# Kernel tuning notes

Hardware: AMD Instinct MI355X
Metric: run time of the kernel (lower is better)

The kernel has to match this reference:

```python
import jax, jax.numpy as jnp
import numpy as np

N, F_IN, H, C, E = 50000, 256, 4, 64, 800000
HC = H * C  # n_target_nodes = 256


def setup_inputs() -> dict:
    key = jax.random.key(0)
    ks = jax.random.split(key, 16)
    s = 1.0 / np.sqrt(F_IN)
    inp = {
        "x": jax.random.normal(ks[0], (N, F_IN), jnp.float32),
        "edge_index": jax.random.randint(ks[1], (2, E), 0, N, jnp.int64),
        "edge_attr": jax.random.uniform(ks[2], (E, 1), jnp.float32),
        "Wq": jax.random.normal(ks[3], (F_IN, HC), jnp.float32) * s,
        "bq": jnp.zeros((HC,), jnp.float32),
        "Wk": jax.random.normal(ks[4], (F_IN, HC), jnp.float32) * s,
        "bk": jnp.zeros((HC,), jnp.float32),
        "Wv": jax.random.normal(ks[5], (F_IN, HC), jnp.float32) * s,
        "bv": jnp.zeros((HC,), jnp.float32),
        "We": jax.random.normal(ks[6], (1, HC), jnp.float32),
        "be": jnp.zeros((HC,), jnp.float32),
        "Wskip": jax.random.normal(ks[7], (F_IN, HC), jnp.float32) * s,
        "bskip": jnp.zeros((HC,), jnp.float32),
        "gn_weight": jnp.ones((HC,), jnp.float32),
        "gn_bias": jnp.zeros((HC,), jnp.float32),
        "gn_mean_scale": jnp.ones((HC,), jnp.float32),
    }
    return inp


def _la_forward(x, edge_index, edge_attr, Wq, bq, Wk, bk, Wv, bv, We, be,
                Wskip, bskip, gn_weight, gn_bias, gn_mean_scale):
    n = x.shape[0]
    src, dst = edge_index[0], edge_index[1]  # message src(j) -> dst(i)
    q = (x @ Wq + bq).reshape(n, H, C)
    k = (x @ Wk + bk).reshape(n, H, C)
    v = (x @ Wv + bv).reshape(n, H, C)
    e = (edge_attr @ We + be).reshape(-1, H, C)  # [E,H,C]

    k_j = k[src] + e                              # [E,H,C]
    alpha = jnp.einsum('ehc,ehc->eh', q[dst], k_j) / jnp.sqrt(jnp.float32(C))
    # edge-softmax over incoming edges of each dst node
    amax = jax.ops.segment_max(alpha, dst, num_segments=n)      # [N,H]
    ex = jnp.exp(alpha - amax[dst])
    denom = jax.ops.segment_sum(ex, dst, num_segments=n)        # [N,H]
    attn = ex / (denom[dst] + 1e-16)                            # [E,H]

    msg = (v[src] + e) * attn[:, :, None]                       # [E,H,C]
    out = jax.ops.segment_sum(msg, dst, num_segments=n).reshape(n, HC)
    out = out + x @ Wskip + bskip                               # root/skip

    # GraphNorm (single graph batch)
    mean = out.mean(axis=0)
    centered = out - gn_mean_scale * mean
    var = (centered * centered).mean(axis=0)
    out = centered / jnp.sqrt(var + 1e-5) * gn_weight + gn_bias

    out = jax.nn.relu(out)
    xt = out.T @ out                                            # [HC,HC]
    xt_min, xt_max = jnp.min(xt), jnp.max(xt)
    xt = (xt - xt_min) / (xt_max - xt_min + 1e-8)
    return xt


def reference(x, edge_index, edge_attr, Wq, bq, Wk, bk, Wv, bv, We, be,
              Wskip, bskip, gn_weight, gn_bias, gn_mean_scale):
    return _la_forward(x, edge_index, edge_attr, Wq, bq, Wk, bk, Wv, bv,
                       We, be, Wskip, bskip, gn_weight, gn_bias, gn_mean_scale)
```

## Files before the change

### kernel.cpp

```cpp
#include <hip/hip_runtime.h>
#include <math.h>


typedef float f32x4 __attribute__((ext_vector_type(4)));
typedef short s16x8 __attribute__((ext_vector_type(8)));

static __device__ __forceinline__ unsigned short f2bf(float f) {
    unsigned int u = __float_as_uint(f);
    unsigned int r = u + 0x7FFFu + ((u >> 16) & 1u);
    return (unsigned short)(r >> 16);
}
static __device__ __forceinline__ float bf2f(unsigned short u) {
    return __uint_as_float(((unsigned int)u) << 16);
}
static __device__ __forceinline__ float blo(unsigned int u) {
    return __uint_as_float(u << 16);
}
static __device__ __forceinline__ float bhi(unsigned int u) {
    return __uint_as_float(u & 0xffff0000u);
}

#define LOG2E_8 0.18033688011112042f

__global__ void la_x2bf(const float* __restrict__ x, unsigned short* __restrict__ xb,
                        int total4)
{
    int i = blockIdx.x * blockDim.x + threadIdx.x;
    int stride = gridDim.x * blockDim.x;
    for (; i < total4; i += stride) {
        float4 v = ((const float4*)x)[i];
        ushort4 o;
        o.x = f2bf(v.x); o.y = f2bf(v.y); o.z = f2bf(v.z); o.w = f2bf(v.w);
        ((ushort4*)xb)[i] = o;
    }
}

__global__ void la_wprep(const float* __restrict__ Wq, const float* __restrict__ Wk,
                         const float* __restrict__ Wv, const float* __restrict__ Ws,
                         const float* __restrict__ bq, const float* __restrict__ bk,
                         const float* __restrict__ bv, const float* __restrict__ bs,
                         unsigned short* __restrict__ wt, float* __restrict__ bcat)
{
    int col = blockIdx.x;
    int m = col >> 8, c = col & 255;
    const float* W = (m == 0) ? Wq : (m == 1) ? Wk : (m == 2) ? Wv : Ws;
    const float* B = (m == 0) ? bq : (m == 1) ? bk : (m == 2) ? bv : bs;
    int t = threadIdx.x;
    wt[(size_t)col * 256 + t] = f2bf(W[(size_t)t * 256 + c]);
    if (t == 0) bcat[col] = B[c];
}

__global__ __launch_bounds__(256) void la_gemm_mfma(
    const unsigned short* __restrict__ xb, const unsigned short* __restrict__ wt,
    const float* __restrict__ bcat,
    unsigned short* __restrict__ qarr, unsigned short* __restrict__ kv,
    unsigned short* __restrict__ skiparr, int n)
{
    __shared__ __align__(16) unsigned short As[128 * 40];
    __shared__ __align__(16) unsigned short Bs[128 * 40];

    const int row0 = blockIdx.x * 128;
    const int col0 = blockIdx.y * 128;
    const int msel = blockIdx.y >> 1;
    const int t = threadIdx.x;
    const int l = t & 63;
    const int w = t >> 6;
    const int wr = w >> 1, wc = w & 1;
    const int l15 = l & 15, l4 = l >> 4;

    f32x4 acc[4][4];
#pragma unroll
    for (int i = 0; i < 4; ++i)
#pragma unroll
        for (int j = 0; j < 4; ++j) acc[i][j] = (f32x4){0.f, 0.f, 0.f, 0.f};

    for (int k0 = 0; k0 < 256; k0 += 32) {
#pragma unroll
        for (int c2 = 0; c2 < 2; ++c2) {
            int chunk = t + c2 * 256;
            int r  = chunk >> 2;
            int ko = (chunk & 3) * 8;
            int ga = row0 + r;
            s16x8 va = (s16x8){0,0,0,0,0,0,0,0};
            if (ga < n) va = *(const s16x8*)(xb + (size_t)ga * 256 + k0 + ko);
            *(s16x8*)(As + r * 40 + ko) = va;
            int gb = col0 + r;
            s16x8 vb = *(const s16x8*)(wt + (size_t)gb * 256 + k0 + ko);
            *(s16x8*)(Bs + r * 40 + ko) = vb;
        }
        __syncthreads();
        s16x8 af[4], bfr[4];
#pragma unroll
        for (int f = 0; f < 4; ++f) {
            af[f]  = *(const s16x8*)(As + (wr * 64 + f * 16 + l15) * 40 + l4 * 8);
            bfr[f] = *(const s16x8*)(Bs + (wc * 64 + f * 16 + l15) * 40 + l4 * 8);
        }
#pragma unroll
        for (int fm = 0; fm < 4; ++fm)
#pragma unroll
            for (int fn = 0; fn < 4; ++fn)
                acc[fm][fn] = __builtin_amdgcn_mfma_f32_16x16x32_bf16(
                    af[fm], bfr[fn], acc[fm][fn], 0, 0, 0);
        __syncthreads();
    }

#pragma unroll
    for (int fm = 0; fm < 4; ++fm) {
#pragma unroll
        for (int fn = 0; fn < 4; ++fn) {
            int gc = col0 + wc * 64 + fn * 16 + l15;
            int c  = gc & 255;
            float bb = bcat[gc];
#pragma unroll
            for (int j = 0; j < 4; ++j) {
                int gr = row0 + wr * 64 + fm * 16 + l4 * 4 + j;
                if (gr >= n) continue;
                unsigned short val = f2bf(acc[fm][fn][j] + bb);
                if (msel == 0) {
                    qarr[(size_t)gr * 256 + c] = val;
                } else if (msel == 3) {
                    skiparr[(size_t)gr * 256 + c] = val;
                } else {
                    int hh = c >> 6, ch = c & 63;
                    size_t idx = (size_t)gr * 512 + hh * 128 + (ch >> 2) * 8
                               + (ch & 3) + ((msel == 2) ? 4 : 0);
                    kv[idx] = val;
                }
            }
        }
    }
}

__global__ void la_hist(const int* __restrict__ dst, int e, int* __restrict__ deg)
{
    int i = blockIdx.x * blockDim.x + threadIdx.x;
    int stride = gridDim.x * blockDim.x;
    for (; i < e; i += stride) atomicAdd(&deg[dst[i]], 1);
}

__global__ void la_chunksum(const int* __restrict__ deg, int n, int* __restrict__ part)
{
    int b = blockIdx.x, t = threadIdx.x;
    int i = b * 256 + t;
    int v = (i < n) ? deg[i] : 0;
#pragma unroll
    for (int mask = 32; mask >= 1; mask >>= 1) v += __shfl_xor(v, mask);
    __shared__ int ws[4];
    if ((t & 63) == 0) ws[t >> 6] = v;
    __syncthreads();
    if (t == 0) part[b] = ws[0] + ws[1] + ws[2] + ws[3];
}

__global__ void la_scanpart(int* __restrict__ part, int nb)
{
    __shared__ int s[256];
    int t = threadIdx.x;
    int v = (t < nb) ? part[t] : 0;
    int orig = v;
    s[t] = v;
    __syncthreads();
    for (int o = 1; o < 256; o <<= 1) {
        int u = (t >= o) ? s[t - o] : 0;
        __syncthreads();
        s[t] += u;
        __syncthreads();
    }
    if (t < nb) part[t] = s[t] - orig;
}

__global__ void la_scanfinal(const int* __restrict__ deg, int n,
                             const int* __restrict__ part, int* __restrict__ offs,
                             int* __restrict__ cursor, int e)
{
    int b = blockIdx.x, t = threadIdx.x;
    int i = b * 256 + t;
    int d = (i < n) ? deg[i] : 0;
    int v = d;
#pragma unroll
    for (int o = 1; o < 64; o <<= 1) {
        int u = __shfl_up(v, o);
        if ((t & 63) >= o) v += u;
    }
    __shared__ int wt[4];
    if ((t & 63) == 63) wt[t >> 6] = v;
    __syncthreads();
    int add = 0;
    for (int wv = 0; wv < (t >> 6); ++wv) add += wt[wv];
    int excl = v + add - d + part[b];
    if (i < n) { offs[i] = excl; cursor[i] = excl; }
    if (b == 0 && t == 0) offs[n] = e;
}

__global__ void la_scatter(const int* __restrict__ src, const int* __restrict__ dst,
                           const float* __restrict__ ea, int e,
                           int* __restrict__ cursor, uint2* __restrict__ rec)
{
    int i = blockIdx.x * blockDim.x + threadIdx.x;
    int stride = gridDim.x * blockDim.x;
    for (; i < e; i += stride) {
        int d = dst[i];
        int pos = atomicAdd(&cursor[d], 1);
        rec[pos] = make_uint2((unsigned int)src[i], __float_as_uint(ea[i]));
    }
}

__global__ __launch_bounds__(256) void la_attn3(
    const unsigned short* __restrict__ qarr,
    const unsigned short* __restrict__ kv,
    const unsigned short* __restrict__ skiparr,
    const uint2* __restrict__ rec,
    const int* __restrict__ offs,
    const float* __restrict__ We, const float* __restrict__ be,
    float* __restrict__ outb)
{
    const int node = blockIdx.x;
    const int t = threadIdx.x;
    const int h = t >> 6;
    const int l = t & 63;
    const int quarter = l >> 4;
    const int lc = l & 15;
    const int cb = h * 64 + lc * 4;

    uint2 qp = *(const uint2*)(qarr + (size_t)node * 256 + cb);
    const float q0 = blo(qp.x), q1 = bhi(qp.x);
    const float q2 = blo(qp.y), q3 = bhi(qp.y);
    float4 we4 = *(const float4*)(We + cb);
    float4 be4 = *(const float4*)(be + cb);

    float pw = fmaf(q3, we4.w, fmaf(q2, we4.z, fmaf(q1, we4.y, q0 * we4.x)));
    float pb = fmaf(q3, be4.w, fmaf(q2, be4.z, fmaf(q1, be4.y, q0 * be4.x)));
#pragma unroll
    for (int mask = 1; mask <= 8; mask <<= 1) {
        pw += __shfl_xor(pw, mask);
        pb += __shfl_xor(pb, mask);
    }
    const float qWe8 = pw * LOG2E_8;
    const float qbe8 = pb * LOG2E_8;

    const int start = offs[node], end = offs[node + 1];
    const int koff = h * 128 + lc * 8;

    float lsum = 0.f, Sfa = 0.f;
    float a0 = 0.f, a1 = 0.f, a2 = 0.f, a3 = 0.f;

    for (int j0 = start; j0 < end; j0 += 4) {
        int j = j0 + quarter;
        bool valid = (j < end);
        int jj = valid ? j : j0;
        uint2 r = rec[jj];
        int   s   = (int)r.x;
        float eaj = __uint_as_float(r.y);
        uint4 kvu = *(const uint4*)(kv + (((size_t)s) << 9) + koff);
        float k0 = blo(kvu.x), k1 = bhi(kvu.x);
        float k2 = blo(kvu.y), k3 = bhi(kvu.y);
        float d = fmaf(q3, k3, fmaf(q2, k2, fmaf(q1, k1, q0 * k0)));
#pragma unroll
        for (int mask = 1; mask <= 8; mask <<= 1) d += __shfl_xor(d, mask);
        float aL = fmaf(d, LOG2E_8, fmaf(eaj, qWe8, qbe8));
        aL = valid ? aL : -INFINITY;
        float f = exp2f(aL);
        lsum += f;
        Sfa = fmaf(f, eaj, Sfa);
        float v0 = blo(kvu.z), v1 = bhi(kvu.z);
        float v2 = blo(kvu.w), v3 = bhi(kvu.w);
        a0 = fmaf(f, v0, a0);
        a1 = fmaf(f, v1, a1);
        a2 = fmaf(f, v2, a2);
        a3 = fmaf(f, v3, a3);
    }

#pragma unroll
    for (int mask = 16; mask <= 32; mask <<= 1) {
        lsum += __shfl_xor(lsum, mask);
        Sfa  += __shfl_xor(Sfa,  mask);
        a0   += __shfl_xor(a0,   mask);
        a1   += __shfl_xor(a1,   mask);
        a2   += __shfl_xor(a2,   mask);
        a3   += __shfl_xor(a3,   mask);
    }

    if (quarter == 0) {
        float inv = 1.f / (lsum + 1e-16f);
        uint2 sp = *(const uint2*)(skiparr + (size_t)node * 256 + cb);
        float4 o;
        o.x = fmaf(we4.x, Sfa, fmaf(be4.x, lsum, a0)) * inv + blo(sp.x);
        o.y = fmaf(we4.y, Sfa, fmaf(be4.y, lsum, a1)) * inv + bhi(sp.x);
        o.z = fmaf(we4.z, Sfa, fmaf(be4.z, lsum, a2)) * inv + blo(sp.y);
        o.w = fmaf(we4.w, Sfa, fmaf(be4.w, lsum, a3)) * inv + bhi(sp.y);
        *(float4*)(outb + (size_t)node * 256 + cb) = o;
    }
}

__global__ __launch_bounds__(256) void la_colsum(
    const float* __restrict__ outb, float* __restrict__ cs,
    float* __restrict__ cs2, int n)
{
    const int col = threadIdx.x;
    const int r0 = blockIdx.x * 64;
    const int rend = (r0 + 64 < n) ? r0 + 64 : n;
    float s = 0.f, s2 = 0.f;
    for (int r = r0; r < rend; ++r) {
        float vv = outb[(size_t)r * 256 + col];
        s += vv;
        s2 = fmaf(vv, vv, s2);
    }
    atomicAdd(&cs[col], s);
    atomicAdd(&cs2[col], s2);
}

__global__ void la_coeff(const float* __restrict__ cs, const float* __restrict__ cs2,
                         const float* __restrict__ gnw, const float* __restrict__ gnb,
                         const float* __restrict__ gms,
                         float* __restrict__ A, float* __restrict__ B, int n)
{
    int j = threadIdx.x;
    float invn = 1.f / (float)n;
    float mean = cs[j] * invn;
    float m2   = cs2[j] * invn;
    float s    = gms[j];
    float var  = m2 - 2.f * s * mean * mean + s * s * mean * mean;
    float inv  = 1.f / sqrtf(var + 1e-5f);
    float a    = gnw[j] * inv;
    A[j] = a;
    B[j] = gnb[j] - s * mean * a;
}

__global__ __launch_bounds__(256) void la_gram_mfma(
    const float* __restrict__ outb, const float* __restrict__ A,
    const float* __restrict__ B, float* __restrict__ xt, int n, int kchunk)
{
    __shared__ __align__(16) unsigned int Ta[128 * 20];
    __shared__ __align__(16) unsigned int Tb[128 * 20];

    const int bx = blockIdx.x;
    const int kc   = bx / 3;
    const int tile = bx - kc * 3;
    const int i0 = (tile == 2) ? 128 : 0;
    const int j0 = (tile == 0) ? 0 : 128;
    const bool diag = (tile != 1);
    const int kbeg = kc * kchunk;
    if (kbeg >= n) return;
    const int kend = (kbeg + kchunk < n) ? kbeg + kchunk : n;

    const int t = threadIdx.x;
    const int l = t & 63, w = t >> 6;
    const int wr = w >> 1, wc = w & 1;
    const int l15 = l & 15, l4 = l >> 4;

    const int kp  = t >> 4;
    const int cg8 = t & 15;

    float Ai[8], Bi[8], Aj[8], Bj[8];
#pragma unroll
    for (int u = 0; u < 2; ++u) {
        float4 a = *(const float4*)(A + i0 + cg8 * 8 + u * 4);
        float4 b = *(const float4*)(B + i0 + cg8 * 8 + u * 4);
        Ai[u*4+0]=a.x; Ai[u*4+1]=a.y; Ai[u*4+2]=a.z; Ai[u*4+3]=a.w;
        Bi[u*4+0]=b.x; Bi[u*4+1]=b.y; Bi[u*4+2]=b.z; Bi[u*4+3]=b.w;
        float4 a2 = *(const float4*)(A + j0 + cg8 * 8 + u * 4);
        float4 b2 = *(const float4*)(B + j0 + cg8 * 8 + u * 4);
        Aj[u*4+0]=a2.x; Aj[u*4+1]=a2.y; Aj[u*4+2]=a2.z; Aj[u*4+3]=a2.w;
        Bj[u*4+0]=b2.x; Bj[u*4+1]=b2.y; Bj[u*4+2]=b2.z; Bj[u*4+3]=b2.w;
    }

    f32x4 acc[4][4];
#pragma unroll
    for (int i = 0; i < 4; ++i)
#pragma unroll
        for (int j = 0; j < 4; ++j) acc[i][j] = (f32x4){0.f, 0.f, 0.f, 0.f};

    const int nsteps = (kend - kbeg + 31) >> 5;
    for (int ks = 0; ks < nsteps; ++ks) {
        const int gr0 = kbeg + ks * 32 + kp * 2;
        const bool v0 = (gr0 < kend), v1 = (gr0 + 1 < kend);

        {
            float r0[8], r1[8];
            float4 xa = make_float4(0,0,0,0), xb4 = make_float4(0,0,0,0);
            float4 ya = make_float4(0,0,0,0), yb4 = make_float4(0,0,0,0);
            if (v0) {
                xa  = *(const float4*)(outb + (size_t)gr0 * 256 + i0 + cg8 * 8);
                xb4 = *(const float4*)(outb + (size_t)gr0 * 256 + i0 + cg8 * 8 + 4);
            }
            if (v1) {
                ya  = *(const float4*)(outb + (size_t)(gr0+1) * 256 + i0 + cg8 * 8);
                yb4 = *(const float4*)(outb + (size_t)(gr0+1) * 256 + i0 + cg8 * 8 + 4);
            }
            float xs[8] = {xa.x,xa.y,xa.z,xa.w,xb4.x,xb4.y,xb4.z,xb4.w};
            float ys[8] = {ya.x,ya.y,ya.z,ya.w,yb4.x,yb4.y,yb4.z,yb4.w};
#pragma unroll
            for (int j = 0; j < 8; ++j) {
                r0[j] = v0 ? fmaxf(fmaf(xs[j], Ai[j], Bi[j]), 0.f) : 0.f;
                r1[j] = v1 ? fmaxf(fmaf(ys[j], Ai[j], Bi[j]), 0.f) : 0.f;
            }
#pragma unroll
            for (int j = 0; j < 8; ++j) {
                int c = cg8 * 8 + j;
                unsigned int u = (unsigned int)f2bf(r0[j])
                               | ((unsigned int)f2bf(r1[j]) << 16);
                Ta[c * 20 + (kp ^ (((c >> 3) & 3) << 2))] = u;
            }
        }
        if (!diag) {
            float r0[8], r1[8];
            float4 xa = make_float4(0,0,0,0), xb4 = make_float4(0,0,0,0);
            float4 ya = make_float4(0,0,0,0), yb4 = make_float4(0,0,0,0);
            if (v0) {
                xa  = *(const float4*)(outb + (size_t)gr0 * 256 + j0 + cg8 * 8);
                xb4 = *(const float4*)(outb + (size_t)gr0 * 256 + j0 + cg8 * 8 + 4);
            }
            if (v1) {
                ya  = *(const float4*)(outb + (size_t)(gr0+1) * 256 + j0 + cg8 * 8);
                yb4 = *(const float4*)(outb + (size_t)(gr0+1) * 256 + j0 + cg8 * 8 + 4);
            }
            float xs[8] = {xa.x,xa.y,xa.z,xa.w,xb4.x,xb4.y,xb4.z,xb4.w};
            float ys[8] = {ya.x,ya.y,ya.z,ya.w,yb4.x,yb4.y,yb4.z,yb4.w};
#pragma unroll
            for (int j = 0; j < 8; ++j) {
                r0[j] = v0 ? fmaxf(fmaf(xs[j], Aj[j], Bj[j]), 0.f) : 0.f;
                r1[j] = v1 ? fmaxf(fmaf(ys[j], Aj[j], Bj[j]), 0.f) : 0.f;
            }
#pragma unroll
            for (int j = 0; j < 8; ++j) {
                int c = cg8 * 8 + j;
                unsigned int u = (unsigned int)f2bf(r0[j])
                               | ((unsigned int)f2bf(r1[j]) << 16);
                Tb[c * 20 + (kp ^ (((c >> 3) & 3) << 2))] = u;
            }
        }
        __syncthreads();

        const unsigned int* TB = diag ? Ta : Tb;
        s16x8 af[4], bfr[4];
#pragma unroll
        for (int f = 0; f < 4; ++f) {
            int ca = wr * 64 + f * 16 + l15;
            af[f] = *(const s16x8*)(Ta + ca * 20 + ((l4 * 4) ^ (((ca >> 3) & 3) << 2)));
            int cb2 = wc * 64 + f * 16 + l15;
            bfr[f] = *(const s16x8*)(TB + cb2 * 20 + ((l4 * 4) ^ (((cb2 >> 3) & 3) << 2)));
        }
#pragma unroll
        for (int fm = 0; fm < 4; ++fm)
#pragma unroll
            for (int fn = 0; fn < 4; ++fn)
                acc[fm][fn] = __builtin_amdgcn_mfma_f32_16x16x32_bf16(
                    af[fm], bfr[fn], acc[fm][fn], 0, 0, 0);
        __syncthreads();
    }

#pragma unroll
    for (int fm = 0; fm < 4; ++fm)
#pragma unroll
        for (int fn = 0; fn < 4; ++fn) {
            int col = j0 + wc * 64 + fn * 16 + l15;
#pragma unroll
            for (int j = 0; j < 4; ++j) {
                int row = i0 + wr * 64 + fm * 16 + l4 * 4 + j;
                float vv = acc[fm][fn][j];
                atomicAdd(&xt[(size_t)row * 256 + col], vv);
                if (tile == 1)
                    atomicAdd(&xt[(size_t)col * 256 + row], vv);
            }
        }
}

__global__ __launch_bounds__(256) void la_minmax_part(
    const float* __restrict__ xt, float* __restrict__ mmp)
{
    const int b = blockIdx.x, t = threadIdx.x;
    float mn = INFINITY, mx = -INFINITY;
#pragma unroll
    for (int k = 0; k < 2; ++k) {
        float4 v = ((const float4*)xt)[b * 512 + k * 256 + t];
        mn = fminf(mn, fminf(fminf(v.x, v.y), fminf(v.z, v.w)));
        mx = fmaxf(mx, fmaxf(fmaxf(v.x, v.y), fmaxf(v.z, v.w)));
    }
#pragma unroll
    for (int mask = 32; mask >= 1; mask >>= 1) {
        mn = fminf(mn, __shfl_xor(mn, mask));
        mx = fmaxf(mx, __shfl_xor(mx, mask));
    }
    __shared__ float smn[4], smx[4];
    if ((t & 63) == 0) { smn[t >> 6] = mn; smx[t >> 6] = mx; }
    __syncthreads();
    if (t == 0) {
        mn = fminf(fminf(smn[0], smn[1]), fminf(smn[2], smn[3]));
        mx = fmaxf(fmaxf(smx[0], smx[1]), fmaxf(smx[2], smx[3]));
        mmp[b * 2]     = mn;
        mmp[b * 2 + 1] = mx;
    }
}

__global__ void la_norm(float* __restrict__ xt, const float* __restrict__ mmp)
{
    float mn = INFINITY, mx = -INFINITY;
#pragma unroll
    for (int i = 0; i < 32; ++i) {
        mn = fminf(mn, mmp[i * 2]);
        mx = fmaxf(mx, mmp[i * 2 + 1]);
    }
    float inv = 1.f / (mx - mn + 1e-8f);
    int i = blockIdx.x * blockDim.x + threadIdx.x;
    xt[i] = (xt[i] - mn) * inv;
}

extern "C" void kernel_launch(void* const* d_in, const int* in_sizes, int n_in,
                              void* d_out, int out_size, void* d_ws, size_t ws_size,
                              hipStream_t stream)
{
    const float* x   = (const float*)d_in[0];
    const int*   ei  = (const int*)  d_in[1];
    const float* ea  = (const float*)d_in[2];
    const float* Wq  = (const float*)d_in[3];
    const float* bq  = (const float*)d_in[4];
    const float* Wk  = (const float*)d_in[5];
    const float* bk  = (const float*)d_in[6];
    const float* Wv  = (const float*)d_in[7];
    const float* bv  = (const float*)d_in[8];
    const float* We  = (const float*)d_in[9];
    const float* be  = (const float*)d_in[10];
    const float* Ws  = (const float*)d_in[11];
    const float* bs  = (const float*)d_in[12];
    const float* gnw = (const float*)d_in[13];
    const float* gnb = (const float*)d_in[14];
    const float* gms = (const float*)d_in[15];

    const int n = in_sizes[0] / 256;
    const int e = in_sizes[1] / 2;
    const int* srcI = ei;
    const int* dstI = ei + e;

    char* ws = (char*)d_ws;
    size_t off = 0;
    auto take = [&](size_t bytes) -> void* {
        void* p = (void*)(ws + off);
        off += (bytes + 255) & ~(size_t)255;
        return p;
    };
    unsigned short* xb    = (unsigned short*)take((size_t)n * 256 * 2);
    unsigned short* wtbuf = (unsigned short*)take((size_t)1024 * 256 * 2);
    float*          bcat  = (float*)take(1024 * 4);
    unsigned short* qarr  = (unsigned short*)take((size_t)n * 256 * 2);
    unsigned short* kv    = (unsigned short*)take((size_t)n * 512 * 2);
    unsigned short* skipb = (unsigned short*)take((size_t)n * 256 * 2);
    float* outb   = (float*)take((size_t)n * 256 * 4);
    int*   deg    = (int*)  take((size_t)n * 4);
    int*   cursor = (int*)  take((size_t)n * 4);
    int*   offs   = (int*)  take((size_t)(n + 1) * 4);
    int*   part   = (int*)  take(256 * 4);
    uint2* csrR   = (uint2*)take((size_t)e * 8);
    float* cs     = (float*)take(256 * 4);
    float* cs2    = (float*)take(256 * 4);
    float* cA     = (float*)take(256 * 4);
    float* cB     = (float*)take(256 * 4);
    float* mmp    = (float*)take(64 * 4);
    (void)ws_size; (void)n_in; (void)out_size;

    float* xt = (float*)d_out;

    hipMemsetAsync(deg, 0, (size_t)n * 4, stream);
    hipMemsetAsync(cs,  0, 256 * 4, stream);
    hipMemsetAsync(cs2, 0, 256 * 4, stream);
    hipMemsetAsync(xt,  0, (size_t)65536 * 4, stream);

    la_x2bf <<<2048, 256, 0, stream>>>(x, xb, n * 64);
    la_wprep<<<1024, 256, 0, stream>>>(Wq, Wk, Wv, Ws, bq, bk, bv, bs, wtbuf, bcat);

    dim3 gg((n + 127) / 128, 8);
    la_gemm_mfma<<<gg, 256, 0, stream>>>(xb, wtbuf, bcat, qarr, kv, skipb, n);

    const int nchunk = (n + 255) / 256;
    la_hist     <<<1024, 256, 0, stream>>>(dstI, e, deg);
    la_chunksum <<<nchunk, 256, 0, stream>>>(deg, n, part);
    la_scanpart <<<1, 256, 0, stream>>>(part, nchunk);
    la_scanfinal<<<nchunk, 256, 0, stream>>>(deg, n, part, offs, cursor, e);
    la_scatter  <<<1024, 256, 0, stream>>>(srcI, dstI, ea, e, cursor, csrR);

    la_attn3<<<n, 256, 0, stream>>>(qarr, kv, skipb, csrR, offs, We, be, outb);

    la_colsum<<<(n + 63) / 64, 256, 0, stream>>>(outb, cs, cs2, n);
    la_coeff <<<1, 256, 0, stream>>>(cs, cs2, gnw, gnb, gms, cA, cB, n);

    const int KSPLIT = 64;
    int kchunk = ((n + KSPLIT - 1) / KSPLIT + 31) & ~31;
    la_gram_mfma<<<3 * KSPLIT, 256, 0, stream>>>(outb, cA, cB, xt, n, kchunk);

    la_minmax_part<<<32, 256, 0, stream>>>(xt, mmp);
    la_norm<<<256, 256, 0, stream>>>(xt, mmp);
}
```

Baseline: 461.4 us.

## Fuse x-to-bf16 conversion into GEMM, store attention output as bf16, fold GraphNorm coeffs

Removes the separate x→bf16 pass by having the projection GEMM load fp32 x rows, convert them and keep a 64-row bf16 tile resident in LDS while looping over all 1024 output columns. The weight transpose is rebuilt as a tiled LDS transpose with far fewer blocks. The attention output buffer becomes bf16, halving traffic for colsum and the Gram kernel, and the GraphNorm coefficient kernel is folded into the Gram kernel. The costs are extra rounding of the pre-norm activations and a GEMM with fewer, longer-running blocks that each restage B tiles eight times.

New measurement: 492.1 us. 1.07x slower.

```diff
diff --git a/kernel.cpp b/kernel.cpp
--- a/kernel.cpp
+++ b/kernel.cpp
@@ -22,109 +22,134 @@
 
 #define LOG2E_8 0.18033688011112042f
 
-__global__ void la_x2bf(const float* __restrict__ x, unsigned short* __restrict__ xb,
-                        int total4)
-{
-    int i = blockIdx.x * blockDim.x + threadIdx.x;
-    int stride = gridDim.x * blockDim.x;
-    for (; i < total4; i += stride) {
-        float4 v = ((const float4*)x)[i];
-        ushort4 o;
-        o.x = f2bf(v.x); o.y = f2bf(v.y); o.z = f2bf(v.z); o.w = f2bf(v.w);
-        ((ushort4*)xb)[i] = o;
-    }
-}
-
-__global__ void la_wprep(const float* __restrict__ Wq, const float* __restrict__ Wk,
-                         const float* __restrict__ Wv, const float* __restrict__ Ws,
-                         const float* __restrict__ bq, const float* __restrict__ bk,
-                         const float* __restrict__ bv, const float* __restrict__ bs,
-                         unsigned short* __restrict__ wt, float* __restrict__ bcat)
-{
-    int col = blockIdx.x;
-    int m = col >> 8, c = col & 255;
+__global__ __launch_bounds__(256) void la_wprep2(
+    const float* __restrict__ Wq, const float* __restrict__ Wk,
+    const float* __restrict__ Wv, const float* __restrict__ Ws,
+    const float* __restrict__ bq, const float* __restrict__ bk,
+    const float* __restrict__ bv, const float* __restrict__ bs,
+    unsigned short* __restrict__ wt, float* __restrict__ bcat)
+{
+    __shared__ float T[64][68];
+    const int bid = blockIdx.x;
+    const int m  = bid >> 4;
+    const int kt = (bid >> 2) & 3, ct = bid & 3;
+    const int k0 = kt * 64, c0 = ct * 64;
     const float* W = (m == 0) ? Wq : (m == 1) ? Wk : (m == 2) ? Wv : Ws;
     const float* B = (m == 0) ? bq : (m == 1) ? bk : (m == 2) ? bv : bs;
-    int t = threadIdx.x;
-    wt[(size_t)col * 256 + t] = f2bf(W[(size_t)t * 256 + c]);
-    if (t == 0) bcat[col] = B[c];
-}
-
-__global__ __launch_bounds__(256) void la_gemm_mfma(
-    const unsigned short* __restrict__ xb, const unsigned short* __restrict__ wt,
+    const int t = threadIdx.x;
+
+#pragma unroll
+    for (int it = 0; it < 4; ++it) {
+        int s = it * 256 + t;
+        int r = s >> 4;
+        int q = (s & 15) * 4;
+        float4 v = *(const float4*)(W + (size_t)(k0 + r) * 256 + c0 + q);
+        T[r][q + 0] = v.x; T[r][q + 1] = v.y;
+        T[r][q + 2] = v.z; T[r][q + 3] = v.w;
+    }
+    __syncthreads();
+#pragma unroll
+    for (int it = 0; it < 4; ++it) {
+        int s = it * 256 + t;
+        int c = s >> 4;
+        int kq = (s & 15) * 4;
+        ushort4 o;
+        o.x = f2bf(T[kq + 0][c]); o.y = f2bf(T[kq + 1][c]);
+        o.z = f2bf(T[kq + 2][c]); o.w = f2bf(T[kq + 3][c]);
+        *(ushort4*)(wt + (size_t)(m * 256 + c0 + c) * 256 + k0 + kq) = o;
+    }
+    if (kt == 0 && t < 64) bcat[m * 256 + c0 + t] = B[c0 + t];
+}
+
+__global__ __launch_bounds__(256) void la_gemm2(
+    const float* __restrict__ x, const unsigned short* __restrict__ wt,
     const float* __restrict__ bcat,
     unsigned short* __restrict__ qarr, unsigned short* __restrict__ kv,
     unsigned short* __restrict__ skiparr, int n)
 {
-    __shared__ __align__(16) unsigned short As[128 * 40];
+    __shared__ __align__(16) unsigned short As[64 * 264];
     __shared__ __align__(16) unsigned short Bs[128 * 40];
 
-    const int row0 = blockIdx.x * 128;
-    const int col0 = blockIdx.y * 128;
-    const int msel = blockIdx.y >> 1;
+    const int row0 = blockIdx.x * 64;
     const int t = threadIdx.x;
-    const int l = t & 63;
-    const int w = t >> 6;
-    const int wr = w >> 1, wc = w & 1;
+    const int l = t & 63, w = t >> 6;
+    const int wr = w & 1, wc = w >> 1;
     const int l15 = l & 15, l4 = l >> 4;
 
-    f32x4 acc[4][4];
-#pragma unroll
-    for (int i = 0; i < 4; ++i)
-#pragma unroll
-        for (int j = 0; j < 4; ++j) acc[i][j] = (f32x4){0.f, 0.f, 0.f, 0.f};
-
-    for (int k0 = 0; k0 < 256; k0 += 32) {
-#pragma unroll
-        for (int c2 = 0; c2 < 2; ++c2) {
-            int chunk = t + c2 * 256;
-            int r  = chunk >> 2;
-            int ko = (chunk & 3) * 8;
-            int ga = row0 + r;
-            s16x8 va = (s16x8){0,0,0,0,0,0,0,0};
-            if (ga < n) va = *(const s16x8*)(xb + (size_t)ga * 256 + k0 + ko);
-            *(s16x8*)(As + r * 40 + ko) = va;
-            int gb = col0 + r;
-            s16x8 vb = *(const s16x8*)(wt + (size_t)gb * 256 + k0 + ko);
-            *(s16x8*)(Bs + r * 40 + ko) = vb;
-        }
-        __syncthreads();
-        s16x8 af[4], bfr[4];
-#pragma unroll
-        for (int f = 0; f < 4; ++f) {
-            af[f]  = *(const s16x8*)(As + (wr * 64 + f * 16 + l15) * 40 + l4 * 8);
-            bfr[f] = *(const s16x8*)(Bs + (wc * 64 + f * 16 + l15) * 40 + l4 * 8);
-        }
-#pragma unroll
-        for (int fm = 0; fm < 4; ++fm)
-#pragma unroll
-            for (int fn = 0; fn < 4; ++fn)
-                acc[fm][fn] = __builtin_amdgcn_mfma_f32_16x16x32_bf16(
-                    af[fm], bfr[fn], acc[fm][fn], 0, 0, 0);
-        __syncthreads();
-    }
-
-#pragma unroll
-    for (int fm = 0; fm < 4; ++fm) {
-#pragma unroll
-        for (int fn = 0; fn < 4; ++fn) {
-            int gc = col0 + wc * 64 + fn * 16 + l15;
-            int c  = gc & 255;
-            float bb = bcat[gc];
-#pragma unroll
-            for (int j = 0; j < 4; ++j) {
-                int gr = row0 + wr * 64 + fm * 16 + l4 * 4 + j;
-                if (gr >= n) continue;
-                unsigned short val = f2bf(acc[fm][fn][j] + bb);
-                if (msel == 0) {
-                    qarr[(size_t)gr * 256 + c] = val;
-                } else if (msel == 3) {
-                    skiparr[(size_t)gr * 256 + c] = val;
-                } else {
-                    int hh = c >> 6, ch = c & 63;
-                    size_t idx = (size_t)gr * 512 + hh * 128 + (ch >> 2) * 8
-                               + (ch & 3) + ((msel == 2) ? 4 : 0);
-                    kv[idx] = val;
+#pragma unroll
+    for (int it = 0; it < 16; ++it) {
+        int s = it * 256 + t;
+        int r = s >> 6;
+        int q = (s & 63) * 4;
+        int gr = row0 + r;
+        float4 v = make_float4(0.f, 0.f, 0.f, 0.f);
+        if (gr < n) v = *(const float4*)(x + (size_t)gr * 256 + q);
+        ushort4 o;
+        o.x = f2bf(v.x); o.y = f2bf(v.y); o.z = f2bf(v.z); o.w = f2bf(v.w);
+        *(ushort4*)(As + r * 264 + q) = o;
+    }
+    __syncthreads();
+
+    for (int p = 0; p < 8; ++p) {
+        const int col0 = p * 128;
+        const int msel = p >> 1;
+        f32x4 acc[2][4];
+#pragma unroll
+        for (int i = 0; i < 2; ++i)
+#pragma unroll
+            for (int j = 0; j < 4; ++j) acc[i][j] = (f32x4){0.f, 0.f, 0.f, 0.f};
+
+        for (int ks = 0; ks < 8; ++ks) {
+            const int k0 = ks * 32;
+#pragma unroll
+            for (int it = 0; it < 2; ++it) {
+                int s = it * 256 + t;
+                int c = s >> 2;
+                int ko = (s & 3) * 8;
+                *(s16x8*)(Bs + c * 40 + ko) =
+                    *(const s16x8*)(wt + (size_t)(col0 + c) * 256 + k0 + ko);
+            }
+            __syncthreads();
+            s16x8 af[2], bfr[4];
+#pragma unroll
+            for (int f = 0; f < 2; ++f)
+                af[f] = *(const s16x8*)(As + (wr * 32 + f * 16 + l15) * 264
+                                        + k0 + l4 * 8);
+#pragma unroll
+            for (int f = 0; f < 4; ++f)
+                bfr[f] = *(const s16x8*)(Bs + (wc * 64 + f * 16 + l15) * 40
+                                         + l4 * 8);
+#pragma unroll
+            for (int fm = 0; fm < 2; ++fm)
+#pragma unroll
+                for (int fn = 0; fn < 4; ++fn)
+                    acc[fm][fn] = __builtin_amdgcn_mfma_f32_16x16x32_bf16(
+                        af[fm], bfr[fn], acc[fm][fn], 0, 0, 0);
+            __syncthreads();
+        }
+
+#pragma unroll
+        for (int fm = 0; fm < 2; ++fm) {
+#pragma unroll
+            for (int fn = 0; fn < 4; ++fn) {
+                int gc = col0 + wc * 64 + fn * 16 + l15;
+                int c  = gc & 255;
+                float bb = bcat[gc];
+#pragma unroll
+                for (int j = 0; j < 4; ++j) {
+                    int gr = row0 + wr * 32 + fm * 16 + l4 * 4 + j;
+                    if (gr >= n) continue;
+                    unsigned short val = f2bf(acc[fm][fn][j] + bb);
+                    if (msel == 0) {
+                        qarr[(size_t)gr * 256 + c] = val;
+                    } else if (msel == 3) {
+                        skiparr[(size_t)gr * 256 + c] = val;
+                    } else {
+                        int hh = c >> 6, ch = c & 63;
+                        size_t idx = (size_t)gr * 512 + hh * 128 + (ch >> 2) * 8
+                                   + (ch & 3) + ((msel == 2) ? 4 : 0);
+                        kv[idx] = val;
+                    }
                 }
             }
         }
@@ -211,7 +236,7 @@
     const uint2* __restrict__ rec,
     const int* __restrict__ offs,
     const float* __restrict__ We, const float* __restrict__ be,
-    float* __restrict__ outb)
+    unsigned short* __restrict__ outb)
 {
     const int node = blockIdx.x;
     const int t = threadIdx.x;
@@ -282,17 +307,17 @@
     if (quarter == 0) {
         float inv = 1.f / (lsum + 1e-16f);
         uint2 sp = *(const uint2*)(skiparr + (size_t)node * 256 + cb);
-        float4 o;
-        o.x = fmaf(we4.x, Sfa, fmaf(be4.x, lsum, a0)) * inv + blo(sp.x);
-        o.y = fmaf(we4.y, Sfa, fmaf(be4.y, lsum, a1)) * inv + bhi(sp.x);
-        o.z = fmaf(we4.z, Sfa, fmaf(be4.z, lsum, a2)) * inv + blo(sp.y);
-        o.w = fmaf(we4.w, Sfa, fmaf(be4.w, lsum, a3)) * inv + bhi(sp.y);
-        *(float4*)(outb + (size_t)node * 256 + cb) = o;
+        ushort4 o;
+        o.x = f2bf(fmaf(we4.x, Sfa, fmaf(be4.x, lsum, a0)) * inv + blo(sp.x));
+        o.y = f2bf(fmaf(we4.y, Sfa, fmaf(be4.y, lsum, a1)) * inv + bhi(sp.x));
+        o.z = f2bf(fmaf(we4.z, Sfa, fmaf(be4.z, lsum, a2)) * inv + blo(sp.y));
+        o.w = f2bf(fmaf(we4.w, Sfa, fmaf(be4.w, lsum, a3)) * inv + bhi(sp.y));
+        *(ushort4*)(outb + (size_t)node * 256 + cb) = o;
     }
 }
 
 __global__ __launch_bounds__(256) void la_colsum(
-    const float* __restrict__ outb, float* __restrict__ cs,
+    const unsigned short* __restrict__ outb, float* __restrict__ cs,
     float* __restrict__ cs2, int n)
 {
     const int col = threadIdx.x;
@@ -300,7 +325,7 @@
     const int rend = (r0 + 64 < n) ? r0 + 64 : n;
     float s = 0.f, s2 = 0.f;
     for (int r = r0; r < rend; ++r) {
-        float vv = outb[(size_t)r * 256 + col];
+        float vv = bf2f(outb[(size_t)r * 256 + col]);
         s += vv;
         s2 = fmaf(vv, vv, s2);
     }
@@ -308,26 +333,12 @@
     atomicAdd(&cs2[col], s2);
 }
 
-__global__ void la_coeff(const float* __restrict__ cs, const float* __restrict__ cs2,
-                         const float* __restrict__ gnw, const float* __restrict__ gnb,
-                         const float* __restrict__ gms,
-                         float* __restrict__ A, float* __restrict__ B, int n)
-{
-    int j = threadIdx.x;
-    float invn = 1.f / (float)n;
-    float mean = cs[j] * invn;
-    float m2   = cs2[j] * invn;
-    float s    = gms[j];
-    float var  = m2 - 2.f * s * mean * mean + s * s * mean * mean;
-    float inv  = 1.f / sqrtf(var + 1e-5f);
-    float a    = gnw[j] * inv;
-    A[j] = a;
-    B[j] = gnb[j] - s * mean * a;
-}
-
 __global__ __launch_bounds__(256) void la_gram_mfma(
-    const float* __restrict__ outb, const float* __restrict__ A,
-    const float* __restrict__ B, float* __restrict__ xt, int n, int kchunk)
+    const unsigned short* __restrict__ outb,
+    const float* __restrict__ cs, const float* __restrict__ cs2,
+    const float* __restrict__ gnw, const float* __restrict__ gnb,
+    const float* __restrict__ gms,
+    float* __restrict__ xt, int n, int kchunk)
 {
     __shared__ __align__(16) unsigned int Ta[128 * 20];
     __shared__ __align__(16) unsigned int Tb[128 * 20];
@@ -350,17 +361,28 @@
     const int kp  = t >> 4;
     const int cg8 = t & 15;
 
+    const float invn = 1.f / (float)n;
     float Ai[8], Bi[8], Aj[8], Bj[8];
 #pragma unroll
-    for (int u = 0; u < 2; ++u) {
-        float4 a = *(const float4*)(A + i0 + cg8 * 8 + u * 4);
-        float4 b = *(const float4*)(B + i0 + cg8 * 8 + u * 4);
-        Ai[u*4+0]=a.x; Ai[u*4+1]=a.y; Ai[u*4+2]=a.z; Ai[u*4+3]=a.w;
-        Bi[u*4+0]=b.x; Bi[u*4+1]=b.y; Bi[u*4+2]=b.z; Bi[u*4+3]=b.w;
-        float4 a2 = *(const float4*)(A + j0 + cg8 * 8 + u * 4);
-        float4 b2 = *(const float4*)(B + j0 + cg8 * 8 + u * 4);
-        Aj[u*4+0]=a2.x; Aj[u*4+1]=a2.y; Aj[u*4+2]=a2.z; Aj[u*4+3]=a2.w;
-        Bj[u*4+0]=b2.x; Bj[u*4+1]=b2.y; Bj[u*4+2]=b2.z; Bj[u*4+3]=b2.w;
+    for (int j = 0; j < 8; ++j) {
+        {
+            int ci = i0 + cg8 * 8 + j;
+            float mean = cs[ci] * invn;
+            float m2   = cs2[ci] * invn;
+            float s    = gms[ci];
+            float var  = m2 - 2.f * s * mean * mean + s * s * mean * mean;
+            float a    = gnw[ci] / sqrtf(var + 1e-5f);
+            Ai[j] = a; Bi[j] = gnb[ci] - s * mean * a;
+        }
+        {
+            int cj = j0 + cg8 * 8 + j;
+            float mean = cs[cj] * invn;
+            float m2   = cs2[cj] * invn;
+            float s    = gms[cj];
+            float var  = m2 - 2.f * s * mean * mean + s * s * mean * mean;
+            float a    = gnw[cj] / sqrtf(var + 1e-5f);
+            Aj[j] = a; Bj[j] = gnb[cj] - s * mean * a;
+        }
     }
 
     f32x4 acc[4][4];
@@ -375,56 +397,38 @@
         const bool v0 = (gr0 < kend), v1 = (gr0 + 1 < kend);
 
         {
-            float r0[8], r1[8];
-            float4 xa = make_float4(0,0,0,0), xb4 = make_float4(0,0,0,0);
-            float4 ya = make_float4(0,0,0,0), yb4 = make_float4(0,0,0,0);
-            if (v0) {
-                xa  = *(const float4*)(outb + (size_t)gr0 * 256 + i0 + cg8 * 8);
-                xb4 = *(const float4*)(outb + (size_t)gr0 * 256 + i0 + cg8 * 8 + 4);
-            }
-            if (v1) {
-                ya  = *(const float4*)(outb + (size_t)(gr0+1) * 256 + i0 + cg8 * 8);
-                yb4 = *(const float4*)(outb + (size_t)(gr0+1) * 256 + i0 + cg8 * 8 + 4);
-            }
-            float xs[8] = {xa.x,xa.y,xa.z,xa.w,xb4.x,xb4.y,xb4.z,xb4.w};
-            float ys[8] = {ya.x,ya.y,ya.z,ya.w,yb4.x,yb4.y,yb4.z,yb4.w};
+            uint4 u0 = make_uint4(0,0,0,0), u1 = make_uint4(0,0,0,0);
+            if (v0) u0 = *(const uint4*)(outb + (size_t)gr0 * 256 + i0 + cg8 * 8);
+            if (v1) u1 = *(const uint4*)(outb + (size_t)(gr0+1) * 256 + i0 + cg8 * 8);
+            float xs[8] = {blo(u0.x),bhi(u0.x),blo(u0.y),bhi(u0.y),
+                           blo(u0.z),bhi(u0.z),blo(u0.w),bhi(u0.w)};
+            float ys[8] = {blo(u1.x),bhi(u1.x),blo(u1.y),bhi(u1.y),
+                           blo(u1.z),bhi(u1.z),blo(u1.w),bhi(u1.w)};
 #pragma unroll
             for (int j = 0; j < 8; ++j) {
-                r0[j] = v0 ? fmaxf(fmaf(xs[j], Ai[j], Bi[j]), 0.f) : 0.f;
-                r1[j] = v1 ? fmaxf(fmaf(ys[j], Ai[j], Bi[j]), 0.f) : 0.f;
-            }
-#pragma unroll
-            for (int j = 0; j < 8; ++j) {
+                float r0 = v0 ? fmaxf(fmaf(xs[j], Ai[j], Bi[j]), 0.f) : 0.f;
+                float r1 = v1 ? fmaxf(fmaf(ys[j], Ai[j], Bi[j]), 0.f) : 0.f;
                 int c = cg8 * 8 + j;
-                unsigned int u = (unsigned int)f2bf(r0[j])
-                               | ((unsigned int)f2bf(r1[j]) << 16);
+                unsigned int u = (unsigned int)f2bf(r0)
+                               | ((unsigned int)f2bf(r1) << 16);
                 Ta[c * 20 + (kp ^ (((c >> 3) & 3) << 2))] = u;
             }
         }
         if (!diag) {
-            float r0[8], r1[8];
-            float4 xa = make_float4(0,0,0,0), xb4 = make_float4(0,0,0,0);
-            float4 ya = make_float4(0,0,0,0), yb4 = make_float4(0,0,0,0);
-            if (v0) {
-                xa  = *(const float4*)(outb + (size_t)gr0 * 256 + j0 + cg8 * 8);
-                xb4 = *(const float4*)(outb + (size_t)gr0 * 256 + j0 + cg8 * 8 + 4);
-            }
-            if (v1) {
-                ya  = *(const float4*)(outb + (size_t)(gr0+1) * 256 + j0 + cg8 * 8);
-                yb4 = *(const float4*)(outb + (size_t)(gr0+1) * 256 + j0 + cg8 * 8 + 4);
-            }
-            float xs[8] = {xa.x,xa.y,xa.z,xa.w,xb4.x,xb4.y,xb4.z,xb4.w};
-            float ys[8] = {ya.x,ya.y,ya.z,ya.w,yb4.x,yb4.y,yb4.z,yb4.w};
+            uint4 u0 = make_uint4(0,0,0,0), u1 = make_uint4(0,0,0,0);
+            if (v0) u0 = *(const uint4*)(outb + (size_t)gr0 * 256 + j0 + cg8 * 8);
+            if (v1) u1 = *(const uint4*)(outb + (size_t)(gr0+1) * 256 + j0 + cg8 * 8);
+            float xs[8] = {blo(u0.x),bhi(u0.x),blo(u0.y),bhi(u0.y),
+                           blo(u0.z),bhi(u0.z),blo(u0.w),bhi(u0.w)};
+            float ys[8] = {blo(u1.x),bhi(u1.x),blo(u1.y),bhi(u1.y),
+                           blo(u1.z),bhi(u1.z),blo(u1.w),bhi(u1.w)};
 #pragma unroll
             for (int j = 0; j < 8; ++j) {
-                r0[j] = v0 ? fmaxf(fmaf(xs[j], Aj[j], Bj[j]), 0.f) : 0.f;
-                r1[j] = v1 ? fmaxf(fmaf(ys[j], Aj[j], Bj[j]), 0.f) : 0.f;
-            }
-#pragma unroll
-            for (int j = 0; j < 8; ++j) {
+                float r0 = v0 ? fmaxf(fmaf(xs[j], Aj[j], Bj[j]), 0.f) : 0.f;
+                float r1 = v1 ? fmaxf(fmaf(ys[j], Aj[j], Bj[j]), 0.f) : 0.f;
                 int c = cg8 * 8 + j;
-                unsigned int u = (unsigned int)f2bf(r0[j])
-                               | ((unsigned int)f2bf(r1[j]) << 16);
+                unsigned int u = (unsigned int)f2bf(r0)
+                               | ((unsigned int)f2bf(r1) << 16);
                 Tb[c * 20 + (kp ^ (((c >> 3) & 3) << 2))] = u;
             }
         }
@@ -537,13 +541,12 @@
         off += (bytes + 255) & ~(size_t)255;
         return p;
     };
-    unsigned short* xb    = (unsigned short*)take((size_t)n * 256 * 2);
     unsigned short* wtbuf = (unsigned short*)take((size_t)1024 * 256 * 2);
     float*          bcat  = (float*)take(1024 * 4);
     unsigned short* qarr  = (unsigned short*)take((size_t)n * 256 * 2);
     unsigned short* kv    = (unsigned short*)take((size_t)n * 512 * 2);
     unsigned short* skipb = (unsigned short*)take((size_t)n * 256 * 2);
-    float* outb   = (float*)take((size_t)n * 256 * 4);
+    unsigned short* outb  = (unsigned short*)take((size_t)n * 256 * 2);
     int*   deg    = (int*)  take((size_t)n * 4);
     int*   cursor = (int*)  take((size_t)n * 4);
     int*   offs   = (int*)  take((size_t)(n + 1) * 4);
@@ -551,8 +554,6 @@
     uint2* csrR   = (uint2*)take((size_t)e * 8);
     float* cs     = (float*)take(256 * 4);
     float* cs2    = (float*)take(256 * 4);
-    float* cA     = (float*)take(256 * 4);
-    float* cB     = (float*)take(256 * 4);
     float* mmp    = (float*)take(64 * 4);
     (void)ws_size; (void)n_in; (void)out_size;
 
@@ -563,11 +564,9 @@
     hipMemsetAsync(cs2, 0, 256 * 4, stream);
     hipMemsetAsync(xt,  0, (size_t)65536 * 4, stream);
 
-    la_x2bf <<<2048, 256, 0, stream>>>(x, xb, n * 64);
-    la_wprep<<<1024, 256, 0, stream>>>(Wq, Wk, Wv, Ws, bq, bk, bv, bs, wtbuf, bcat);
-
-    dim3 gg((n + 127) / 128, 8);
-    la_gemm_mfma<<<gg, 256, 0, stream>>>(xb, wtbuf, bcat, qarr, kv, skipb, n);
+    la_wprep2<<<64, 256, 0, stream>>>(Wq, Wk, Wv, Ws, bq, bk, bv, bs, wtbuf, bcat);
+    la_gemm2 <<<(n + 63) / 64, 256, 0, stream>>>(x, wtbuf, bcat,
+                                                 qarr, kv, skipb, n);
 
     const int nchunk = (n + 255) / 256;
     la_hist     <<<1024, 256, 0, stream>>>(dstI, e, deg);
@@ -579,11 +578,11 @@
     la_attn3<<<n, 256, 0, stream>>>(qarr, kv, skipb, csrR, offs, We, be, outb);
 
     la_colsum<<<(n + 63) / 64, 256, 0, stream>>>(outb, cs, cs2, n);
-    la_coeff <<<1, 256, 0, stream>>>(cs, cs2, gnw, gnb, gms, cA, cB, n);
 
     const int KSPLIT = 64;
     int kchunk = ((n + KSPLIT - 1) / KSPLIT + 31) & ~31;
-    la_gram_mfma<<<3 * KSPLIT, 256, 0, stream>>>(outb, cA, cB, xt, n, kchunk);
+    la_gram_mfma<<<3 * KSPLIT, 256, 0, stream>>>(outb, cs, cs2, gnw, gnb, gms,
+                                                 xt, n, kchunk);
 
     la_minmax_part<<<32, 256, 0, stream>>>(xt, mmp);
     la_norm<<<256, 256, 0, stream>>>(xt, mmp);
```
